# Optimization experiments

Hardware: AMD Instinct MI355X
Metric: run time of the kernel (lower is better)

## Reference

```python
import jax, jax.numpy as jnp
import numpy as np

N, M, NTYPES, C, AXIS = 4096, 128, 2, 64, 16
TYPE_IDX = (0, 2048, 4096)        # atom-type partition along center axis
NTYPE_IDX = (0, 64, 128)          # neighbor-type partition along neighbor axis
RCUT = 6.0
BOX = 20.0
SR_MEAN = (0.1, 0.1)              # precomputed stats (get_stats)
SR_STD = (0.05, 0.05)
NORM = 20.0                       # avg neighbor count + 1


def setup_inputs() -> dict:
    key = jax.random.key(0)
    ks = jax.random.split(key, 16)
    coord_3N = jax.random.uniform(ks[0], (3, N), dtype=jnp.float32) * BOX
    box = jnp.full((3,), BOX, dtype=jnp.float32)
    # neighbors sorted by type: first 64 of type 0, last 64 of type 1
    nbr0 = jax.random.randint(ks[1], (N, M // 2), 0, TYPE_IDX[1])
    nbr1 = jax.random.randint(ks[2], (N, M // 2), TYPE_IDX[1], TYPE_IDX[2])
    nbrs_idx = jnp.concatenate([nbr0, nbr1], axis=1).astype(jnp.int32)
    # 4 per-(center,neighbor)-type embedding nets, widths 1->16->32->64, stacked
    eW0 = jax.random.normal(ks[3], (4, 1, 16), dtype=jnp.float32)
    eb0 = jax.random.normal(ks[4], (4, 16), dtype=jnp.float32) * 0.1
    eW1 = jax.random.normal(ks[5], (4, 16, 32), dtype=jnp.float32) / 4.0
    eb1 = jax.random.normal(ks[6], (4, 32), dtype=jnp.float32) * 0.1
    eW2 = jax.random.normal(ks[7], (4, 32, 64), dtype=jnp.float32) / (32.0 ** 0.5)
    eb2 = jax.random.normal(ks[8], (4, 64), dtype=jnp.float32) * 0.1
    Tbias = jnp.zeros((1, C), dtype=jnp.float32)
    # 2 per-type fitting nets, widths 1024->128->128->1, stacked
    fW0 = jax.random.normal(ks[9], (2, AXIS * C, 128), dtype=jnp.float32) / (AXIS * C) ** 0.5
    fb0 = jnp.zeros((2, 128), dtype=jnp.float32)
    fW1 = jax.random.normal(ks[10], (2, 128, 128), dtype=jnp.float32) / (128.0 ** 0.5)
    fb1 = jnp.zeros((2, 128), dtype=jnp.float32)
    fW2 = jax.random.normal(ks[11], (2, 128, 1), dtype=jnp.float32) / (128.0 ** 0.5)
    fb2 = jnp.zeros((2, 1), dtype=jnp.float32)
    Ebias = jnp.zeros((2,), dtype=jnp.float32)
    return {"coord_3N": coord_3N, "box": box, "nbrs_idx": nbrs_idx,
            "eW0": eW0, "eb0": eb0, "eW1": eW1, "eb1": eb1, "eW2": eW2, "eb2": eb2,
            "Tbias": Tbias, "fW0": fW0, "fb0": fb0, "fW1": fW1, "fb1": fb1,
            "fW2": fW2, "fb2": fb2, "Ebias": Ebias}


def reference(coord_3N, box, nbrs_idx, eW0, eb0, eW1, eb1, eW2, eb2,
              Tbias, fW0, fb0, fW1, fb1, fW2, fb2, Ebias):
    # --- neighbor gather + minimal-image relative coords (get_relative_coord) ---
    x_3NM = coord_3N[:, nbrs_idx] - coord_3N[:, :, None]            # [3,N,M]
    x_3NM = x_3NM - box[:, None, None] * jnp.round(x_3NM / box[:, None, None])
    r2 = (x_3NM ** 2).sum(0)
    mask = r2 > 1e-12
    rsafe = jnp.sqrt(jnp.where(mask, r2, 1.0))                      # safe for grads
    r_NM = jnp.where(mask, rsafe, 0.0)                              # [N,M]
    # --- smooth radial feature sr(r) = switch(r)/r ---
    sw = 0.5 * jnp.cos(jnp.pi * jnp.minimum(r_NM, RCUT) / RCUT) + 0.5
    sr_NM = jnp.where(mask & (r_NM < RCUT), sw / rsafe, 0.0)
    # --- per-center-type normalization (slice_t / concat_t over type_idx) ---
    srn_rows, srcn = [], []
    for i in range(NTYPES):
        blk = sr_NM[TYPE_IDX[i]:TYPE_IDX[i + 1]]
        srn_rows.append(blk / SR_STD[i])
        srcn.append((blk - SR_MEAN[i]) / SR_STD[i])
    sr_norm_NM = jnp.concatenate(srn_rows, 0)
    x_norm_3NM = x_3NM / jnp.where(mask, rsafe, 1.0)[None]
    R_3NM = 3 ** 0.5 * sr_norm_NM * x_norm_3NM
    R2diag_3NM = 9 ** 0.5 * sr_norm_NM * (x_norm_3NM ** 2 - 1.0 / 3.0)
    R2offd_3NM = 18 ** 0.5 * sr_norm_NM * (x_norm_3NM * jnp.stack([x_norm_3NM[1], x_norm_3NM[2], x_norm_3NM[0]]))
    R_XNM = jnp.concatenate([sr_norm_NM[None], R_3NM, R2diag_3NM, R2offd_3NM])  # [10,N,M]

    # --- per-(center,neighbor)-type embedding MLPs on scalar sr feature ---
    def embed(x, k):  # x: [n, m] -> [n, m, C]
        h = jnp.tanh(x[:, :, None] @ eW0[k] + eb0[k])
        h = jnp.tanh(h @ eW1[k] + eb1[k])
        return jnp.tanh(h @ eW2[k] + eb2[k])

    rows = []
    for i in range(NTYPES):
        cols = [embed(srcn[i][:, NTYPE_IDX[j]:NTYPE_IDX[j + 1]], i * NTYPES + j)
                for j in range(NTYPES)]
        rows.append(jnp.concatenate(cols, 1))
    embed_NMC = jnp.concatenate(rows, 0)                            # [N,M,C]

    # --- descriptor contraction ---
    T_NXC = jnp.einsum('xnm,nmc->nxc', R_XNM, embed_NMC) / NORM     # [N,10,C]
    T_NC = T_NXC[:, 0] + Tbias
    T_N3C = T_NXC[:, 1:4]
    T_N6C = T_NXC[:, 4:]
    G_NAC = T_NC[:, None] * T_NC[:, :AXIS, None] \
        + (T_N3C[:, :, None] * T_N3C[:, :, :AXIS, None]).sum(1)     # [N,AXIS,C]
    # use_2nd branch
    G1 = T_N3C[:, :, AXIS:2 * AXIS]                                 # [N,3,AXIS]
    G11 = jnp.concatenate([G1 ** 2,
                           2 ** 0.5 * G1 * jnp.stack([G1[:, 1], G1[:, 2], G1[:, 0]], axis=1)], axis=1)
    G2 = G11 + T_N6C[:, :, AXIS:2 * AXIS]                           # [N,6,AXIS]
    G_NAC = G_NAC + jnp.einsum('nxa,nxc->nac', G2, T_N6C)

    # --- per-type fitting nets ---
    Gflat = G_NAC.reshape(N, AXIS * C)
    energy = jnp.zeros((), dtype=Gflat.dtype)
    for t in range(NTYPES):
        g = Gflat[TYPE_IDX[t]:TYPE_IDX[t + 1]]
        h = jnp.tanh(g @ fW0[t] + fb0[t])
        h = jnp.tanh(h @ fW1[t] + fb1[t])
        f = h @ fW2[t] + fb2[t]
        energy = energy + (f + Ebias[t]).sum()
    return energy
```

## Files before the change

### kernel.cpp

```cpp
#include <hip/hip_runtime.h>
#include <hip/hip_fp16.h>

typedef _Float16 h16;
typedef h16 v2h __attribute__((ext_vector_type(2)));
typedef h16 v8h __attribute__((ext_vector_type(8)));
typedef float f4 __attribute__((ext_vector_type(4)));

#define NATOM 4096
#define HALF_N 2048
#define K2 2.885390081777927f
#define GSCL 0.015625f
#define W0SCL (64.0f * K2)

#define TBL_N 2048
#define W0MIN_ (-0.201f)
#define DW_ (1.2005f / 2047.0f)
#define RSCALE_ (2047.0f / 1.2005f)

__device__ __forceinline__ float rcp_fast(float x) {
#if __has_builtin(__builtin_amdgcn_rcpf)
  return __builtin_amdgcn_rcpf(x);
#else
  return 1.0f / x;
#endif
}

__device__ __forceinline__ float exp2_fast(float x) {
#if __has_builtin(__builtin_amdgcn_exp2f)
  return __builtin_amdgcn_exp2f(x);
#else
  return exp2f(x);
#endif
}

__device__ __forceinline__ float tanh_e2(float d) {
  float r = rcp_fast(1.0f + exp2_fast(d));
  return fmaf(-2.0f, r, 1.0f);
}

__global__ __launch_bounds__(256) void k_setup(
    const float* __restrict__ eW0, const float* __restrict__ eb0,
    const float* __restrict__ eW1, const float* __restrict__ eb1,
    const float* __restrict__ eW2, const float* __restrict__ eb2,
    const float* __restrict__ fW0,
    h16* __restrict__ tbl, h16* __restrict__ W0t)
{
  const int bid = blockIdx.x, tid = threadIdx.x;
  if (bid < 512) {
    __shared__ float sW1[512];
    __shared__ float sW2[2048];
    __shared__ float sW0s[16], sb0s[16], sb1s[32], sb2s[64];
    const int net = bid >> 7;
    for (int i = tid; i < 512; i += 256) sW1[i] = eW1[net * 512 + i];
    for (int i = tid; i < 2048; i += 256) sW2[i] = eW2[net * 2048 + i];
    if (tid < 16) { sW0s[tid] = eW0[net * 16 + tid]; sb0s[tid] = eb0[net * 16 + tid]; }
    else if (tid >= 32 && tid < 64) sb1s[tid - 32] = eb1[net * 32 + tid - 32];
    else if (tid >= 64 && tid < 128) sb2s[tid - 64] = eb2[net * 64 + tid - 64];
    __syncthreads();

    const int u = (bid & 127) * 256 + tid;
    const int e = u >> 4, cq = u & 15;
    const float w = W0MIN_ + (float)e * DW_;
    const float s = 8.0f * w * rcp_fast(1.0f - fabsf(w));
    float h0[16];
#pragma unroll
    for (int i = 0; i < 16; ++i)
      h0[i] = tanh_e2(K2 * fmaf(s, sW0s[i], sb0s[i]));
    float h1[32];
#pragma unroll
    for (int j = 0; j < 32; ++j) {
      float a = sb1s[j];
#pragma unroll
      for (int i = 0; i < 16; ++i) a = fmaf(h0[i], sW1[i * 32 + j], a);
      h1[j] = tanh_e2(K2 * a);
    }
    f4 a4 = *(const f4*)&sb2s[cq * 4];
    for (int j = 0; j < 32; ++j) {
      f4 wv4 = *(const f4*)&sW2[j * 64 + cq * 4];
      a4 += h1[j] * wv4;
    }
    union { h16 e4[4]; unsigned long long q; } o;
#pragma unroll
    for (int q = 0; q < 4; ++q) o.e4[q] = (h16)tanh_e2(K2 * a4[q]);
    *(unsigned long long*)&tbl[((size_t)(net * TBL_N + e)) * 64 + cq * 4] = o.q;
  } else {
    int idx = (bid - 512) * 256 + tid;
    int t = idx >> 14, n = idx & 127, k8 = (idx >> 7) & 127;
    union { v8h v; h16 e[8]; } o;
#pragma unroll
    for (int i = 0; i < 8; ++i)
      o.e[i] = (h16)(W0SCL * fW0[(size_t)t * 131072 + (size_t)(k8 * 8 + i) * 128 + n]);
    *(v8h*)&W0t[((size_t)t * 128 + n) * 1024 + k8 * 8] = o.v;
  }
}

__global__ __launch_bounds__(256, 3) void k_embed(
    const float* __restrict__ coord, const float* __restrict__ box,
    const int* __restrict__ nbrs, const float* __restrict__ Tbias,
    const h16* __restrict__ tbl, h16* __restrict__ Gout)
{
  __shared__ h16   E32t[4][64][40] __attribute__((aligned(16)));
  __shared__ h16   Rls[4][10][136] __attribute__((aligned(16)));
  __shared__ float Tls[4][10][64];
  __shared__ unsigned int ifx[4][128];

  const int tid = threadIdx.x;
  const int wv = tid >> 6;
  const int lane = tid & 63;
  const int n = blockIdx.x * 4 + wv;
  const int ti = (n >= HALF_N) ? 1 : 0;
  const int c15 = lane & 15, g4 = lane >> 4;

  {
    const float bx = box[0], by = box[1], bz = box[2];
    const float rbx = rcp_fast(bx), rby = rcp_fast(by), rbz = rcp_fast(bz);
    const float cx = coord[n], cy = coord[NATOM + n], cz = coord[2 * NATOM + n];
#pragma unroll
    for (int nb = 0; nb < 2; ++nb) {
      const int m = nb * 64 + lane;
      const int j = nbrs[(size_t)n * 128 + m];
      float dx = coord[j] - cx;
      float dy = coord[NATOM + j] - cy;
      float dz = coord[2 * NATOM + j] - cz;
      dx -= bx * rintf(dx * rbx);
      dy -= by * rintf(dy * rby);
      dz -= bz * rintf(dz * rbz);
      float r2 = dx * dx + dy * dy + dz * dz;
      bool mk = r2 > 1e-12f;
      float rs = sqrtf(mk ? r2 : 1.0f);
      float r  = mk ? rs : 0.0f;
      float sw = 0.5f * __cosf(0.52359878f * fminf(r, 6.0f)) + 0.5f;
      float invr = mk ? rcp_fast(rs) : 1.0f;
      float sr = (mk && r < 6.0f) ? sw * invr : 0.0f;
      float x0 = dx * invr, x1 = dy * invr, x2 = dz * invr;
      float srn = sr * 20.0f;
      float s   = (sr - 0.1f) * 20.0f;
      Rls[wv][0][m] = (h16)srn;
      Rls[wv][1][m] = (h16)(1.7320508f * srn * x0);
      Rls[wv][2][m] = (h16)(1.7320508f * srn * x1);
      Rls[wv][3][m] = (h16)(1.7320508f * srn * x2);
      Rls[wv][4][m] = (h16)(3.0f * srn * (x0 * x0 - 0.33333334f));
      Rls[wv][5][m] = (h16)(3.0f * srn * (x1 * x1 - 0.33333334f));
      Rls[wv][6][m] = (h16)(3.0f * srn * (x2 * x2 - 0.33333334f));
      Rls[wv][7][m] = (h16)(4.2426407f * srn * (x0 * x1));
      Rls[wv][8][m] = (h16)(4.2426407f * srn * (x1 * x2));
      Rls[wv][9][m] = (h16)(4.2426407f * srn * (x2 * x0));
      float wr = s * rcp_fast(8.0f + fabsf(s));
      float fidx = (wr - W0MIN_) * RSCALE_;
      fidx = fminf(fmaxf(fidx, 0.0f), 2045.99f);
      float i0f = floorf(fidx);
      h16 frh = (h16)(fidx - i0f);
      ifx[wv][m] = ((unsigned int)i0f << 16) |
                   (unsigned int)__builtin_bit_cast(unsigned short, frh);
    }
  }

  f4 tac[4];
#pragma unroll
  for (int nt = 0; nt < 4; ++nt) tac[nt] = (f4){0.f, 0.f, 0.f, 0.f};
  const int rrow = (c15 < 10) ? c15 : 9;
  const v8h vzero = {};

  for (int ks = 0; ks < 4; ++ks) {
    {
      const int mloc = lane >> 1, h = lane & 1;
      const int m = ks * 32 + mloc;
      const unsigned int u = ifx[wv][m];
      const int i0 = (int)(u >> 16);
      const h16 fh = __builtin_bit_cast(h16, (unsigned short)(u & 0xffffu));
      v2h fr2; fr2.x = fh; fr2.y = fh;
      const int net = ti * 2 + (m >> 6);
      const h16* rp = tbl + ((size_t)(net * TBL_N + i0)) * 64 + h * 32;
      union U8 { v8h v; v2h p[4]; h16 e[8]; };
      U8 r0[4], r1[4];
#pragma unroll
      for (int q = 0; q < 4; ++q) {
        r0[q].v = *(const v8h*)(rp + q * 8);
        r1[q].v = *(const v8h*)(rp + 64 + q * 8);
      }
      h16 ev[32];
#pragma unroll
      for (int q = 0; q < 4; ++q) {
#pragma unroll
        for (int p = 0; p < 4; ++p) {
          v2h d = r1[q].p[p] - r0[q].p[p];
          v2h e2 = r0[q].p[p] + fr2 * d;
          ev[q * 8 + p * 2]     = e2.x;
          ev[q * 8 + p * 2 + 1] = e2.y;
        }
      }
#pragma unroll
      for (int i = 0; i < 32; ++i)
        E32t[wv][h * 32 + i][mloc] = ev[i];
    }
    {
      v8h ra = *(const v8h*)&Rls[wv][rrow][ks * 32 + g4 * 8];
      if (c15 >= 10) ra = vzero;
#pragma unroll
      for (int nt = 0; nt < 4; ++nt) {
        v8h bf = *(const v8h*)&E32t[wv][nt * 16 + c15][g4 * 8];
        tac[nt] = __builtin_amdgcn_mfma_f32_16x16x32_f16(ra, bf, tac[nt], 0, 0, 0);
      }
    }
  }

#pragma unroll
  for (int nt = 0; nt < 4; ++nt)
#pragma unroll
    for (int r = 0; r < 4; ++r) {
      int x = g4 * 4 + r;
      if (x < 10) Tls[wv][x][nt * 16 + c15] = tac[nt][r] * 0.05f;
    }

  {
    const int c = lane;
    const float tnc  = Tls[wv][0][c] + Tbias[c];
    const float t3c0 = Tls[wv][1][c], t3c1 = Tls[wv][2][c], t3c2 = Tls[wv][3][c];
    const float t6c0 = Tls[wv][4][c], t6c1 = Tls[wv][5][c], t6c2 = Tls[wv][6][c];
    const float t6c3 = Tls[wv][7][c], t6c4 = Tls[wv][8][c], t6c5 = Tls[wv][9][c];
    h16* gp = Gout + (size_t)n * 1024;
#pragma unroll
    for (int a = 0; a < 16; ++a) {
      float g = tnc * (Tls[wv][0][a] + Tbias[a]);
      g += t3c0 * Tls[wv][1][a] + t3c1 * Tls[wv][2][a] + t3c2 * Tls[wv][3][a];
      const float g1x = Tls[wv][1][16 + a], g1y = Tls[wv][2][16 + a], g1z = Tls[wv][3][16 + a];
      g += (g1x * g1x + Tls[wv][4][16 + a]) * t6c0;
      g += (g1y * g1y + Tls[wv][5][16 + a]) * t6c1;
      g += (g1z * g1z + Tls[wv][6][16 + a]) * t6c2;
      g += (1.4142135f * g1x * g1y + Tls[wv][7][16 + a]) * t6c3;
      g += (1.4142135f * g1y * g1z + Tls[wv][8][16 + a]) * t6c4;
      g += (1.4142135f * g1z * g1x + Tls[wv][9][16 + a]) * t6c5;
      gp[a * 64 + c] = (h16)(g * GSCL);
    }
  }
}

__device__ __forceinline__ v8h lds_v8h(const h16* base, int byte) {
  return *(const v8h*)((const char*)base + byte);
}

__global__ __launch_bounds__(256, 2) void k_fit0(
    const h16* __restrict__ G16, const h16* __restrict__ W0t,
    float* __restrict__ P)
{
  __shared__ h16 As[64][64]  __attribute__((aligned(16)));
  __shared__ h16 Bts[128][64] __attribute__((aligned(16)));
  const int tid = threadIdx.x;
  const int atile = blockIdx.x >> 2;
  const int ks = blockIdx.x & 3;
  const int abase = atile * 64;
  const int kbase = ks * 256;
  const int t = (abase >= HALF_N) ? 1 : 0;
  const int lane = tid & 63, w = tid >> 6;
  const int c15 = lane & 15, g4 = lane >> 4;

  f4 acc[8];
#pragma unroll
  for (int nt = 0; nt < 8; ++nt) acc[nt] = (f4){0.f, 0.f, 0.f, 0.f};

  for (int kc = 0; kc < 4; ++kc) {
    const int kb = kbase + kc * 64;
    __syncthreads();
#pragma unroll
    for (int u = 0; u < 2; ++u) {
      int idx = u * 256 + tid;
      int r = idx >> 3, c8 = idx & 7;
      v8h v = *(const v8h*)&G16[(size_t)(abase + r) * 1024 + kb + c8 * 8];
      int byte = r * 128 + ((c8 * 16) ^ ((r & 7) << 4));
      *(v8h*)((char*)&As[0][0] + byte) = v;
    }
#pragma unroll
    for (int u = 0; u < 4; ++u) {
      int idx = u * 256 + tid;
      int nr = idx >> 3, c8 = idx & 7;
      v8h v = *(const v8h*)&W0t[((size_t)t * 128 + nr) * 1024 + kb + c8 * 8];
      int byte = nr * 128 + ((c8 * 16) ^ ((nr & 7) << 4));
      *(v8h*)((char*)&Bts[0][0] + byte) = v;
    }
    __syncthreads();
#pragma unroll
    for (int ksub = 0; ksub < 2; ++ksub) {
      const int ar = 16 * w + c15;
      const int koff = (ksub * 32 + g4 * 8) * 2;
      v8h a = lds_v8h(&As[0][0], ar * 128 + (koff ^ ((ar & 7) << 4)));
#pragma unroll
      for (int nt = 0; nt < 8; ++nt) {
        const int br = nt * 16 + c15;
        v8h b = lds_v8h(&Bts[0][0], br * 128 + (koff ^ ((br & 7) << 4)));
        acc[nt] = __builtin_amdgcn_mfma_f32_16x16x32_f16(a, b, acc[nt], 0, 0, 0);
      }
    }
  }

  float* Pk = P + (size_t)ks * 4096 * 128;
#pragma unroll
  for (int nt = 0; nt < 8; ++nt)
#pragma unroll
    for (int r = 0; r < 4; ++r)
      Pk[(size_t)(abase + 16 * w + g4 * 4 + r) * 128 + nt * 16 + c15] = acc[nt][r];
}

__global__ __launch_bounds__(256, 4) void k_fit1(
    const float* __restrict__ P,
    const float* __restrict__ fb0, const float* __restrict__ fW1,
    const float* __restrict__ fb1, const float* __restrict__ fW2,
    const float* __restrict__ fb2, const float* __restrict__ Ebias,
    float* __restrict__ BP)
{
  __shared__ float ht[128][12];
  __shared__ float Ws1[32][128];
  __shared__ float red[8][33];
  const int tid = threadIdx.x;
  const int abase = blockIdx.x * 8;
  const int t = (abase >= HALF_N) ? 1 : 0;

  {
    const int a = tid >> 5, j0 = (tid & 31) * 4;
    f4 s = K2 * (*(const f4*)&fb0[t * 128 + j0]);
#pragma unroll
    for (int ks = 0; ks < 4; ++ks)
      s += *(const f4*)&P[((size_t)ks * 4096 + abase + a) * 128 + j0];
    ht[j0 + 0][a] = tanh_e2(s.x);
    ht[j0 + 1][a] = tanh_e2(s.y);
    ht[j0 + 2][a] = tanh_e2(s.z);
    ht[j0 + 3][a] = tanh_e2(s.w);
  }

  const int ab = tid & 7, jb = tid >> 3;
  const int j0g = jb * 4;
  f4 acc = K2 * (*(const f4*)&fb1[t * 128 + j0g]);
  for (int kc = 0; kc < 4; ++kc) {
    __syncthreads();
#pragma unroll
    for (int u = 0; u < 2; ++u) {
      int idx = (u * 256 + tid) * 8;
      int kk = idx >> 7, j = idx & 127;
      *(f4*)&Ws1[kk][j] =
          K2 * (*(const f4*)&fW1[(size_t)t * 16384 + (size_t)(kc * 32 + kk) * 128 + j]);
      *(f4*)&Ws1[kk][j + 4] =
          K2 * (*(const f4*)&fW1[(size_t)t * 16384 + (size_t)(kc * 32 + kk) * 128 + j + 4]);
    }
    __syncthreads();
    for (int kk = 0; kk < 32; ++kk) {
      float av = ht[kc * 32 + kk][ab];
      f4 w = *(const f4*)&Ws1[kk][j0g];
      acc += av * w;
    }
  }

  float f = tanh_e2(acc.x) * fW2[t * 128 + j0g + 0]
          + tanh_e2(acc.y) * fW2[t * 128 + j0g + 1]
          + tanh_e2(acc.z) * fW2[t * 128 + j0g + 2]
          + tanh_e2(acc.w) * fW2[t * 128 + j0g + 3];
  red[ab][jb] = f;
  __syncthreads();
  if (tid < 64) {
    const int a = tid & 7, j4 = tid >> 3;
    float v = red[a][j4 * 4] + red[a][j4 * 4 + 1]
            + red[a][j4 * 4 + 2] + red[a][j4 * 4 + 3];
    v += __shfl_xor(v, 32);
    v += __shfl_xor(v, 16);
    v += __shfl_xor(v, 8);
    v += __shfl_xor(v, 4);
    v += __shfl_xor(v, 2);
    v += __shfl_xor(v, 1);
    if (tid == 0) BP[blockIdx.x] = v + 8.0f * (fb2[t] + Ebias[t]);
  }
}

__global__ __launch_bounds__(64) void k_reduce(const float* __restrict__ BP,
                                               float* __restrict__ out)
{
  int tid = threadIdx.x;
  float s = 0.0f;
#pragma unroll
  for (int u = 0; u < 8; ++u) s += BP[tid + 64 * u];
  s += __shfl_xor(s, 32);
  s += __shfl_xor(s, 16);
  s += __shfl_xor(s, 8);
  s += __shfl_xor(s, 4);
  s += __shfl_xor(s, 2);
  s += __shfl_xor(s, 1);
  if (tid == 0) out[0] = s;
}

extern "C" void kernel_launch(void* const* d_in, const int* in_sizes, int n_in,
                              void* d_out, int out_size, void* d_ws, size_t ws_size,
                              hipStream_t stream) {
  const float* coord = (const float*)d_in[0];
  const float* box   = (const float*)d_in[1];
  const int*   nbrs  = (const int*)d_in[2];
  const float* eW0   = (const float*)d_in[3];
  const float* eb0   = (const float*)d_in[4];
  const float* eW1   = (const float*)d_in[5];
  const float* eb1   = (const float*)d_in[6];
  const float* eW2   = (const float*)d_in[7];
  const float* eb2   = (const float*)d_in[8];
  const float* Tbias = (const float*)d_in[9];
  const float* fW0   = (const float*)d_in[10];
  const float* fb0   = (const float*)d_in[11];
  const float* fW1   = (const float*)d_in[12];
  const float* fb1   = (const float*)d_in[13];
  const float* fW2   = (const float*)d_in[14];
  const float* fb2   = (const float*)d_in[15];
  const float* Ebias = (const float*)d_in[16];

  h16*   G16 = (h16*)d_ws;
  float* P   = (float*)((char*)d_ws + (size_t)8 * 1024 * 1024);
  h16*   W0t = (h16*)((char*)d_ws + (size_t)16 * 1024 * 1024);
  float* BP  = (float*)((char*)d_ws + (size_t)17 * 1024 * 1024);
  h16*   tbl = (h16*)((char*)d_ws + (size_t)18 * 1024 * 1024);

  k_setup<<<640, 256, 0, stream>>>(eW0, eb0, eW1, eb1, eW2, eb2, fW0, tbl, W0t);
  k_embed<<<1024, 256, 0, stream>>>(coord, box, nbrs, Tbias, tbl, G16);
  k_fit0<<<256, 256, 0, stream>>>(G16, W0t, P);
  k_fit1<<<512, 256, 0, stream>>>(P, fb0, fW1, fb1, fW2, fb2, Ebias, BP);
  k_reduce<<<1, 64, 0, stream>>>(BP, (float*)d_out);
}
```

Baseline: 48.53 us.

## Pack coords, double-buffer table loads in embed, halve fit0 tile size

Setup gains extra blocks that pack the SoA coordinates into float4, so each neighbor gather in the embed kernel becomes one 16-byte load instead of three scattered loads. The embed kernel drops the LDS index buffer, keeps the packed table index in registers and shares it across lanes with ds_bpermute. It also double-buffers the interpolation-table loads so the next chunk's global reads overlap the current chunk's interpolation and MFMA work. The fit0 GEMM moves to 32-row tiles with a 2x2 wave split, doubling the grid to 512 blocks for better occupancy, at the cost of reloading the W0 tiles in more blocks and using more registers for the buffers.

```diff
diff --git a/kernel.cpp b/kernel.cpp
--- a/kernel.cpp
+++ b/kernel.cpp
@@ -38,12 +38,16 @@
   return fmaf(-2.0f, r, 1.0f);
 }
 
+__device__ __forceinline__ v8h lds_v8h(const h16* base, int byte) {
+  return *(const v8h*)((const char*)base + byte);
+}
+
 __global__ __launch_bounds__(256) void k_setup(
     const float* __restrict__ eW0, const float* __restrict__ eb0,
     const float* __restrict__ eW1, const float* __restrict__ eb1,
     const float* __restrict__ eW2, const float* __restrict__ eb2,
-    const float* __restrict__ fW0,
-    h16* __restrict__ tbl, h16* __restrict__ W0t)
+    const float* __restrict__ fW0, const float* __restrict__ coord,
+    h16* __restrict__ tbl, h16* __restrict__ W0t, f4* __restrict__ coordP)
 {
   const int bid = blockIdx.x, tid = threadIdx.x;
   if (bid < 512) {
@@ -83,7 +87,7 @@
 #pragma unroll
     for (int q = 0; q < 4; ++q) o.e4[q] = (h16)tanh_e2(K2 * a4[q]);
     *(unsigned long long*)&tbl[((size_t)(net * TBL_N + e)) * 64 + cq * 4] = o.q;
-  } else {
+  } else if (bid < 640) {
     int idx = (bid - 512) * 256 + tid;
     int t = idx >> 14, n = idx & 127, k8 = (idx >> 7) & 127;
     union { v8h v; h16 e[8]; } o;
@@ -91,18 +95,23 @@
     for (int i = 0; i < 8; ++i)
       o.e[i] = (h16)(W0SCL * fW0[(size_t)t * 131072 + (size_t)(k8 * 8 + i) * 128 + n]);
     *(v8h*)&W0t[((size_t)t * 128 + n) * 1024 + k8 * 8] = o.v;
+  } else {
+    int idx = (bid - 640) * 256 + tid;
+    f4 c;
+    c.x = coord[idx]; c.y = coord[NATOM + idx]; c.z = coord[2 * NATOM + idx];
+    c.w = 0.0f;
+    coordP[idx] = c;
   }
 }
 
 __global__ __launch_bounds__(256, 3) void k_embed(
-    const float* __restrict__ coord, const float* __restrict__ box,
+    const f4* __restrict__ coordP, const float* __restrict__ box,
     const int* __restrict__ nbrs, const float* __restrict__ Tbias,
     const h16* __restrict__ tbl, h16* __restrict__ Gout)
 {
   __shared__ h16   E32t[4][64][40] __attribute__((aligned(16)));
   __shared__ h16   Rls[4][10][136] __attribute__((aligned(16)));
   __shared__ float Tls[4][10][64];
-  __shared__ unsigned int ifx[4][128];
 
   const int tid = threadIdx.x;
   const int wv = tid >> 6;
@@ -110,18 +119,23 @@
   const int n = blockIdx.x * 4 + wv;
   const int ti = (n >= HALF_N) ? 1 : 0;
   const int c15 = lane & 15, g4 = lane >> 4;
-
+  const int mloc = lane >> 1, hh = lane & 1;
+
+  const int jnb0 = nbrs[(size_t)n * 128 + lane];
+  const int jnb1 = nbrs[(size_t)n * 128 + 64 + lane];
+
+  int uf0 = 0, uf1 = 0;
   {
     const float bx = box[0], by = box[1], bz = box[2];
     const float rbx = rcp_fast(bx), rby = rcp_fast(by), rbz = rcp_fast(bz);
-    const float cx = coord[n], cy = coord[NATOM + n], cz = coord[2 * NATOM + n];
+    const f4 cme = coordP[n];
 #pragma unroll
     for (int nb = 0; nb < 2; ++nb) {
       const int m = nb * 64 + lane;
-      const int j = nbrs[(size_t)n * 128 + m];
-      float dx = coord[j] - cx;
-      float dy = coord[NATOM + j] - cy;
-      float dz = coord[2 * NATOM + j] - cz;
+      const f4 cj = coordP[nb ? jnb1 : jnb0];
+      float dx = cj.x - cme.x;
+      float dy = cj.y - cme.y;
+      float dz = cj.z - cme.z;
       dx -= bx * rintf(dx * rbx);
       dy -= by * rintf(dy * rby);
       dz -= bz * rintf(dz * rbz);
@@ -150,59 +164,65 @@
       fidx = fminf(fmaxf(fidx, 0.0f), 2045.99f);
       float i0f = floorf(fidx);
       h16 frh = (h16)(fidx - i0f);
-      ifx[wv][m] = ((unsigned int)i0f << 16) |
-                   (unsigned int)__builtin_bit_cast(unsigned short, frh);
-    }
-  }
-
-  f4 tac[4];
-#pragma unroll
-  for (int nt = 0; nt < 4; ++nt) tac[nt] = (f4){0.f, 0.f, 0.f, 0.f};
+      int uf = ((int)i0f << 16) |
+               (int)__builtin_bit_cast(unsigned short, frh);
+      if (nb == 0) uf0 = uf; else uf1 = uf;
+    }
+  }
+
+  union U8 { v8h v; v2h p[4]; h16 e[8]; };
   const int rrow = (c15 < 10) ? c15 : 9;
   const v8h vzero = {};
-
-  for (int ks = 0; ks < 4; ++ks) {
-    {
-      const int mloc = lane >> 1, h = lane & 1;
-      const int m = ks * 32 + mloc;
-      const unsigned int u = ifx[wv][m];
-      const int i0 = (int)(u >> 16);
-      const h16 fh = __builtin_bit_cast(h16, (unsigned short)(u & 0xffffu));
-      v2h fr2; fr2.x = fh; fr2.y = fh;
-      const int net = ti * 2 + (m >> 6);
-      const h16* rp = tbl + ((size_t)(net * TBL_N + i0)) * 64 + h * 32;
-      union U8 { v8h v; v2h p[4]; h16 e[8]; };
-      U8 r0[4], r1[4];
-#pragma unroll
-      for (int q = 0; q < 4; ++q) {
-        r0[q].v = *(const v8h*)(rp + q * 8);
-        r1[q].v = *(const v8h*)(rp + 64 + q * 8);
+  f4 tac[4];
+#pragma unroll
+  for (int nt = 0; nt < 4; ++nt) tac[nt] = (f4){0.f, 0.f, 0.f, 0.f};
+
+  auto issue = [&](int ks, U8* buf) -> float {
+    unsigned uu = (unsigned)__builtin_amdgcn_ds_bpermute(
+        (((ks & 1) * 32) + mloc) * 4, (ks < 2) ? uf0 : uf1);
+    int i0 = (int)(uu >> 16);
+    float fr = (float)__builtin_bit_cast(h16, (unsigned short)(uu & 0xffffu));
+    const int net = ti * 2 + (ks >> 1);
+    const h16* rp = tbl + ((size_t)net * TBL_N + i0) * 64 + hh * 8;
+#pragma unroll
+    for (int q = 0; q < 4; ++q) {
+      buf[q].v     = *(const v8h*)(rp + q * 16);
+      buf[4 + q].v = *(const v8h*)(rp + 64 + q * 16);
+    }
+    return fr;
+  };
+
+  auto proc = [&](int ks, U8* buf, float fr) {
+    v2h fr2; fr2.x = (h16)fr; fr2.y = (h16)fr;
+#pragma unroll
+    for (int q = 0; q < 4; ++q) {
+#pragma unroll
+      for (int p = 0; p < 4; ++p) {
+        v2h d = buf[4 + q].p[p] - buf[q].p[p];
+        v2h e2 = buf[q].p[p] + fr2 * d;
+        const int ch = q * 16 + hh * 8 + p * 2;
+        E32t[wv][ch][mloc]     = e2.x;
+        E32t[wv][ch + 1][mloc] = e2.y;
       }
-      h16 ev[32];
-#pragma unroll
-      for (int q = 0; q < 4; ++q) {
-#pragma unroll
-        for (int p = 0; p < 4; ++p) {
-          v2h d = r1[q].p[p] - r0[q].p[p];
-          v2h e2 = r0[q].p[p] + fr2 * d;
-          ev[q * 8 + p * 2]     = e2.x;
-          ev[q * 8 + p * 2 + 1] = e2.y;
-        }
-      }
-#pragma unroll
-      for (int i = 0; i < 32; ++i)
-        E32t[wv][h * 32 + i][mloc] = ev[i];
-    }
-    {
-      v8h ra = *(const v8h*)&Rls[wv][rrow][ks * 32 + g4 * 8];
-      if (c15 >= 10) ra = vzero;
-#pragma unroll
-      for (int nt = 0; nt < 4; ++nt) {
-        v8h bf = *(const v8h*)&E32t[wv][nt * 16 + c15][g4 * 8];
-        tac[nt] = __builtin_amdgcn_mfma_f32_16x16x32_f16(ra, bf, tac[nt], 0, 0, 0);
-      }
-    }
-  }
+    }
+    v8h ra = *(const v8h*)&Rls[wv][rrow][ks * 32 + g4 * 8];
+    if (c15 >= 10) ra = vzero;
+#pragma unroll
+    for (int nt = 0; nt < 4; ++nt) {
+      v8h bf = *(const v8h*)&E32t[wv][nt * 16 + c15][g4 * 8];
+      tac[nt] = __builtin_amdgcn_mfma_f32_16x16x32_f16(ra, bf, tac[nt], 0, 0, 0);
+    }
+  };
+
+  U8 bA[8], bB[8];
+  float frA = issue(0, bA);
+  float frB = issue(1, bB);
+  proc(0, bA, frA);
+  frA = issue(2, bA);
+  proc(1, bB, frB);
+  frB = issue(3, bB);
+  proc(2, bA, frA);
+  proc(3, bB, frB);
 
 #pragma unroll
   for (int nt = 0; nt < 4; ++nt)
@@ -235,36 +255,31 @@
   }
 }
 
-__device__ __forceinline__ v8h lds_v8h(const h16* base, int byte) {
-  return *(const v8h*)((const char*)base + byte);
-}
-
 __global__ __launch_bounds__(256, 2) void k_fit0(
     const h16* __restrict__ G16, const h16* __restrict__ W0t,
     float* __restrict__ P)
 {
-  __shared__ h16 As[64][64]  __attribute__((aligned(16)));
+  __shared__ h16 As[32][64]  __attribute__((aligned(16)));
   __shared__ h16 Bts[128][64] __attribute__((aligned(16)));
   const int tid = threadIdx.x;
-  const int atile = blockIdx.x >> 2;
+  const int tile = blockIdx.x >> 2;
   const int ks = blockIdx.x & 3;
-  const int abase = atile * 64;
+  const int abase = tile * 32;
   const int kbase = ks * 256;
   const int t = (abase >= HALF_N) ? 1 : 0;
   const int lane = tid & 63, w = tid >> 6;
   const int c15 = lane & 15, g4 = lane >> 4;
-
-  f4 acc[8];
-#pragma unroll
-  for (int nt = 0; nt < 8; ++nt) acc[nt] = (f4){0.f, 0.f, 0.f, 0.f};
+  const int mrow = (w & 1) * 16, nh = (w >> 1) * 64;
+
+  f4 acc[4];
+#pragma unroll
+  for (int nt = 0; nt < 4; ++nt) acc[nt] = (f4){0.f, 0.f, 0.f, 0.f};
 
   for (int kc = 0; kc < 4; ++kc) {
     const int kb = kbase + kc * 64;
     __syncthreads();
-#pragma unroll
-    for (int u = 0; u < 2; ++u) {
-      int idx = u * 256 + tid;
-      int r = idx >> 3, c8 = idx & 7;
+    {
+      int r = tid >> 3, c8 = tid & 7;
       v8h v = *(const v8h*)&G16[(size_t)(abase + r) * 1024 + kb + c8 * 8];
       int byte = r * 128 + ((c8 * 16) ^ ((r & 7) << 4));
       *(v8h*)((char*)&As[0][0] + byte) = v;
@@ -280,12 +295,12 @@
     __syncthreads();
 #pragma unroll
     for (int ksub = 0; ksub < 2; ++ksub) {
-      const int ar = 16 * w + c15;
+      const int ar = mrow + c15;
       const int koff = (ksub * 32 + g4 * 8) * 2;
       v8h a = lds_v8h(&As[0][0], ar * 128 + (koff ^ ((ar & 7) << 4)));
 #pragma unroll
-      for (int nt = 0; nt < 8; ++nt) {
-        const int br = nt * 16 + c15;
+      for (int nt = 0; nt < 4; ++nt) {
+        const int br = nh + nt * 16 + c15;
         v8h b = lds_v8h(&Bts[0][0], br * 128 + (koff ^ ((br & 7) << 4)));
         acc[nt] = __builtin_amdgcn_mfma_f32_16x16x32_f16(a, b, acc[nt], 0, 0, 0);
       }
@@ -294,10 +309,10 @@
 
   float* Pk = P + (size_t)ks * 4096 * 128;
 #pragma unroll
-  for (int nt = 0; nt < 8; ++nt)
+  for (int nt = 0; nt < 4; ++nt)
 #pragma unroll
     for (int r = 0; r < 4; ++r)
-      Pk[(size_t)(abase + 16 * w + g4 * 4 + r) * 128 + nt * 16 + c15] = acc[nt][r];
+      Pk[(size_t)(abase + mrow + g4 * 4 + r) * 128 + nh + nt * 16 + c15] = acc[nt][r];
 }
 
 __global__ __launch_bounds__(256, 4) void k_fit1(
@@ -410,10 +425,12 @@
   h16*   W0t = (h16*)((char*)d_ws + (size_t)16 * 1024 * 1024);
   float* BP  = (float*)((char*)d_ws + (size_t)17 * 1024 * 1024);
   h16*   tbl = (h16*)((char*)d_ws + (size_t)18 * 1024 * 1024);
-
-  k_setup<<<640, 256, 0, stream>>>(eW0, eb0, eW1, eb1, eW2, eb2, fW0, tbl, W0t);
-  k_embed<<<1024, 256, 0, stream>>>(coord, box, nbrs, Tbias, tbl, G16);
-  k_fit0<<<256, 256, 0, stream>>>(G16, W0t, P);
+  f4*    cP  = (f4*)((char*)d_ws + (size_t)19 * 1024 * 1024);
+
+  k_setup<<<656, 256, 0, stream>>>(eW0, eb0, eW1, eb1, eW2, eb2, fW0, coord,
+                                   tbl, W0t, cP);
+  k_embed<<<1024, 256, 0, stream>>>(cP, box, nbrs, Tbias, tbl, G16);
+  k_fit0<<<512, 256, 0, stream>>>(G16, W0t, P);
   k_fit1<<<512, 256, 0, stream>>>(P, fb0, fW1, fb1, fW2, fb2, Ebias, BP);
   k_reduce<<<1, 64, 0, stream>>>(BP, (float*)d_out);
 }
```

Result: faster. 45.87 us (-5.5%).
